# Kernel tuning notes

Measured on AMD Instinct MI355X. Metric: run time of the kernel, lower is better.

## Reference

```python
import jax, jax.numpy as jnp
import numpy as np

B = 50000      # batch of target nodes
N = 200000     # total nodes in feature table
K = 32         # sampled neighbors per node
F = 256        # feature dim
F_OUT = 256    # output dim


def setup_inputs() -> dict:
    key = jax.random.key(0)
    k1, k2, k3, k4, k5 = jax.random.split(key, 5)
    x_self = jax.random.normal(k1, (B, F), dtype=jnp.float32)
    feats = jax.random.normal(k2, (N, F), dtype=jnp.float32)
    neigh_idx = jax.random.randint(k3, (B, K), 0, N, dtype=jnp.int64)
    # Linear(2F -> F_OUT), stored as (in, out) for x @ W
    W = jax.random.normal(k4, (F_OUT, 2 * F), dtype=jnp.float32) * (1.0 / np.sqrt(2 * F))
    W = W.T  # (2F, F_OUT)
    b = jax.random.normal(k5, (F_OUT,), dtype=jnp.float32) * 0.01
    return {"x_self": x_self, "feats": feats, "neigh_idx": neigh_idx, "W": W, "b": b}


def reference(x_self, feats, neigh_idx, W, b):
    # gather neighbor features: [B, K, F]
    neigh_feats = feats[neigh_idx]
    # MeanAggregator: mean over neighbor axis (-2)
    x_neigh = neigh_feats.mean(axis=-2)            # [B, F]
    # concat=True path: cat([x_self, x_neigh], axis=1) -> [B, 2F]
    h = jnp.concatenate([x_self, x_neigh], axis=1)
    # Linear layer
    return h @ W + b                                # [B, F_OUT]
```

## Files before the change

### kernel.cpp

```cpp
#include <hip/hip_runtime.h>
#include <hip/hip_bf16.h>
#include <stdint.h>

#define NB 50000
#define NN 200000
#define KN 32
#define FD 256
#define F2 512
#define FO 256

typedef __attribute__((ext_vector_type(8))) short short8v;
typedef __attribute__((ext_vector_type(4))) short short4v;
typedef __attribute__((ext_vector_type(4))) float floatx4;
typedef __attribute__((ext_vector_type(2))) float float2v;

__device__ inline short f2bf(float f) {
    __hip_bfloat16 h = __float2bfloat16(f);
    return *reinterpret_cast<short*>(&h);
}

__global__ void k_quant_feats(const float* __restrict__ feats,
                              unsigned char* __restrict__ Q) {
    long t = (long)blockIdx.x * blockDim.x + threadIdx.x;
    long base = t * 8;
    const float4* src = (const float4*)(feats + base);
    float4 a = src[0], b = src[1];
    int lo = 0, hi = 0;
    lo = __builtin_amdgcn_cvt_pk_fp8_f32(a.x, a.y, lo, false);
    lo = __builtin_amdgcn_cvt_pk_fp8_f32(a.z, a.w, lo, true);
    hi = __builtin_amdgcn_cvt_pk_fp8_f32(b.x, b.y, hi, false);
    hi = __builtin_amdgcn_cvt_pk_fp8_f32(b.z, b.w, hi, true);
    int2 o = { lo, hi };
    *(int2*)(Q + base) = o;
}

__global__ void k_swizzle_W(const float* __restrict__ W,
                            __hip_bfloat16* __restrict__ Wsw) {
    int u = blockIdx.x * blockDim.x + threadIdx.x;
    if (u >= 16384) return;
    int l  = u & 63;
    int tl = (u >> 6) & 3;
    int c  = (u >> 8) & 15;
    int h  = (u >> 12) & 3;
    int n  = (h * 4 + tl) * 16 + (l & 15);
    int kb = c * 32 + (l >> 4) * 8;
    short o[8];
#pragma unroll
    for (int j = 0; j < 8; ++j)
        o[j] = f2bf(W[(long)(kb + j) * FO + n]);
    *(short8v*)((short*)Wsw + (long)u * 8) = *(short8v*)o;
}

__global__ void k_gather_mean(const unsigned char* __restrict__ Q,
                              const float* __restrict__ x_self,
                              const int* __restrict__ idx,
                              __hip_bfloat16* __restrict__ H) {
    int wave = threadIdx.x >> 6;
    int lane = threadIdx.x & 63;
    int b = blockIdx.x * 4 + wave;
    int c4 = lane * 4;

    float4 xs = *(const float4*)(x_self + (long)b * FD + c4);
    short so[4] = { f2bf(xs.x), f2bf(xs.y), f2bf(xs.z), f2bf(xs.w) };
    *(short4v*)((short*)H + (long)b * F2 + c4) = *(short4v*)so;

    const int* ib = idx + (long)b * KN;
    float ax = 0.f, ay = 0.f, az = 0.f, aw = 0.f;
#pragma unroll
    for (int k = 0; k < KN; ++k) {
        int id = ib[k];
        int v = *(const int*)(Q + (long)id * FD + c4);
        float2v lo = __builtin_amdgcn_cvt_pk_f32_fp8(v, false);
        float2v hi = __builtin_amdgcn_cvt_pk_f32_fp8(v, true);
        ax += lo.x; ay += lo.y; az += hi.x; aw += hi.y;
    }
    const float s = 1.0f / (float)KN;
    short o[4] = { f2bf(ax * s), f2bf(ay * s), f2bf(az * s), f2bf(aw * s) };
    *(short4v*)((short*)H + (long)b * F2 + FD + c4) = *(short4v*)o;
}

__global__ void __launch_bounds__(256, 2)
k_gemm(const __hip_bfloat16* __restrict__ H,
       const __hip_bfloat16* __restrict__ Wsw,
       const float* __restrict__ bias,
       float* __restrict__ out) {
    __shared__ char lB[64 * 1024];

    int tid  = threadIdx.x;
    int wave = tid >> 6;
    int lane = tid & 63;
    int cl   = lane & 15;
    int quad = lane >> 4;
    int kq   = quad * 8;

    int h  = blockIdx.x & 3;
    int rt = blockIdx.x >> 2;

    const char* gsrc = (const char*)Wsw + (long)h * 65536;
#pragma unroll
    for (int i = 0; i < 16; ++i) {
        int off = i * 4096 + wave * 1024;
        __builtin_amdgcn_global_load_lds(
            (__attribute__((address_space(1))) void*)(gsrc + off + lane * 16),
            (__attribute__((address_space(3))) void*)(lB + off),
            16, 0, 0);
    }
    __syncthreads();

    int mf = rt * 256 + wave * 64;

    floatx4 acc[4][4];
#pragma unroll
    for (int f = 0; f < 4; ++f)
#pragma unroll
        for (int t = 0; t < 4; ++t) acc[f][t] = (floatx4)(0.f);

    const short8v* lb = (const short8v*)lB;
    for (int c = 0; c < 16; ++c) {
        short8v a[4];
#pragma unroll
        for (int f = 0; f < 4; ++f) {
            long r = min(mf + f * 16 + cl, NB - 1);
            a[f] = *(const short8v*)((const short*)H + r * F2 + c * 32 + kq);
        }
#pragma unroll
        for (int t = 0; t < 4; ++t) {
            short8v bf = lb[(c * 4 + t) * 64 + lane];
#pragma unroll
            for (int f = 0; f < 4; ++f)
                acc[f][t] = __builtin_amdgcn_mfma_f32_16x16x32_bf16(a[f], bf, acc[f][t], 0, 0, 0);
        }
    }

#pragma unroll
    for (int t = 0; t < 4; ++t) {
        int n = h * 64 + t * 16 + cl;
        float bv = bias[n];
#pragma unroll
        for (int f = 0; f < 4; ++f) {
            int row = mf + f * 16 + quad * 4;
#pragma unroll
            for (int r = 0; r < 4; ++r) {
                if (row + r < NB)
                    out[(long)(row + r) * FO + n] = acc[f][t][r] + bv;
            }
        }
    }
}

extern "C" void kernel_launch(void* const* d_in, const int* in_sizes, int n_in,
                              void* d_out, int out_size, void* d_ws, size_t ws_size,
                              hipStream_t stream) {
    const float* x_self = (const float*)d_in[0];
    const float* feats  = (const float*)d_in[1];
    const int*   idx    = (const int*)d_in[2];
    const float* W      = (const float*)d_in[3];
    const float* bias   = (const float*)d_in[4];
    float* out = (float*)d_out;

    unsigned char*  Q   = (unsigned char*)d_ws;
    __hip_bfloat16* H   = (__hip_bfloat16*)((char*)d_ws + (size_t)NN * FD);
    __hip_bfloat16* Wsw = (__hip_bfloat16*)((char*)d_ws + (size_t)NN * FD
                                                        + (size_t)NB * F2 * 2);

    k_quant_feats<<<NN * FD / 8 / 256, 256, 0, stream>>>(feats, Q);
    k_swizzle_W<<<64, 256, 0, stream>>>(W, Wsw);
    k_gather_mean<<<NB / 4, 256, 0, stream>>>(Q, x_self, idx, H);
    k_gemm<<<4 * ((NB + 255) / 256), 256, 0, stream>>>(H, Wsw, bias, out);
}
```

Baseline: 440.3 us.

## Fuse x_self conversion into GEMM, widen gather loads, drop LDS weight staging

The gather kernel now writes only the neighbor-mean half in bf16. Each lane loads 16 fp8 bytes per neighbor across four neighbors in parallel, and the partial sums are reduced with cross-lane shuffles. The GEMM reads x_self in fp32 and converts it to bf16 inline, which removes the intermediate write and read of that half of H. Each 64-row block now covers all 256 output columns and streams the swizzled weights straight from global or cache instead of staging them in LDS. The cost is 128 accumulator registers per thread, less weight reuse per load, and repeated weight traffic through L2.

```diff
diff --git a/kernel.cpp b/kernel.cpp
--- a/kernel.cpp
+++ b/kernel.cpp
@@ -38,106 +38,127 @@
                             __hip_bfloat16* __restrict__ Wsw) {
     int u = blockIdx.x * blockDim.x + threadIdx.x;
     if (u >= 16384) return;
-    int l  = u & 63;
-    int tl = (u >> 6) & 3;
-    int c  = (u >> 8) & 15;
-    int h  = (u >> 12) & 3;
-    int n  = (h * 4 + tl) * 16 + (l & 15);
-    int kb = c * 32 + (l >> 4) * 8;
+    int c = u >> 10;
+    int t = (u >> 6) & 15;
+    int l = u & 63;
+    int kq = (l >> 4) * 8;
+    int n  = t * 16 + (l & 15);
     short o[8];
 #pragma unroll
     for (int j = 0; j < 8; ++j)
-        o[j] = f2bf(W[(long)(kb + j) * FO + n]);
+        o[j] = f2bf(W[(long)(c * 32 + kq + j) * FO + n]);
     *(short8v*)((short*)Wsw + (long)u * 8) = *(short8v*)o;
 }
 
 __global__ void k_gather_mean(const unsigned char* __restrict__ Q,
-                              const float* __restrict__ x_self,
                               const int* __restrict__ idx,
-                              __hip_bfloat16* __restrict__ H) {
+                              __hip_bfloat16* __restrict__ Hn) {
     int wave = threadIdx.x >> 6;
     int lane = threadIdx.x & 63;
     int b = blockIdx.x * 4 + wave;
-    int c4 = lane * 4;
-
-    float4 xs = *(const float4*)(x_self + (long)b * FD + c4);
-    short so[4] = { f2bf(xs.x), f2bf(xs.y), f2bf(xs.z), f2bf(xs.w) };
-    *(short4v*)((short*)H + (long)b * F2 + c4) = *(short4v*)so;
+    int cl   = lane & 15;
+    int quad = lane >> 4;
 
     const int* ib = idx + (long)b * KN;
-    float ax = 0.f, ay = 0.f, az = 0.f, aw = 0.f;
+    float2v acc2[8];
 #pragma unroll
-    for (int k = 0; k < KN; ++k) {
-        int id = ib[k];
-        int v = *(const int*)(Q + (long)id * FD + c4);
-        float2v lo = __builtin_amdgcn_cvt_pk_f32_fp8(v, false);
-        float2v hi = __builtin_amdgcn_cvt_pk_f32_fp8(v, true);
-        ax += lo.x; ay += lo.y; az += hi.x; aw += hi.y;
+    for (int j = 0; j < 8; ++j) acc2[j] = (float2v)(0.f);
+
+#pragma unroll
+    for (int k = 0; k < 8; ++k) {
+        int nid = ib[4 * k + quad];
+        int4 v = *(const int4*)(Q + (long)nid * FD + cl * 16);
+        acc2[0] += __builtin_amdgcn_cvt_pk_f32_fp8(v.x, false);
+        acc2[1] += __builtin_amdgcn_cvt_pk_f32_fp8(v.x, true);
+        acc2[2] += __builtin_amdgcn_cvt_pk_f32_fp8(v.y, false);
+        acc2[3] += __builtin_amdgcn_cvt_pk_f32_fp8(v.y, true);
+        acc2[4] += __builtin_amdgcn_cvt_pk_f32_fp8(v.z, false);
+        acc2[5] += __builtin_amdgcn_cvt_pk_f32_fp8(v.z, true);
+        acc2[6] += __builtin_amdgcn_cvt_pk_f32_fp8(v.w, false);
+        acc2[7] += __builtin_amdgcn_cvt_pk_f32_fp8(v.w, true);
     }
+
+#pragma unroll
+    for (int j = 0; j < 8; ++j) {
+        acc2[j].x += __shfl_xor(acc2[j].x, 16);
+        acc2[j].y += __shfl_xor(acc2[j].y, 16);
+        acc2[j].x += __shfl_xor(acc2[j].x, 32);
+        acc2[j].y += __shfl_xor(acc2[j].y, 32);
+    }
+
+    float2v p0 = (quad & 1) ? acc2[2] : acc2[0];
+    float2v p1 = (quad & 1) ? acc2[3] : acc2[1];
+    float2v q0 = (quad & 1) ? acc2[6] : acc2[4];
+    float2v q1 = (quad & 1) ? acc2[7] : acc2[5];
+    float2v s0 = (quad & 2) ? q0 : p0;
+    float2v s1 = (quad & 2) ? q1 : p1;
     const float s = 1.0f / (float)KN;
-    short o[4] = { f2bf(ax * s), f2bf(ay * s), f2bf(az * s), f2bf(aw * s) };
-    *(short4v*)((short*)H + (long)b * F2 + FD + c4) = *(short4v*)o;
+    short o[4] = { f2bf(s0.x * s), f2bf(s0.y * s), f2bf(s1.x * s), f2bf(s1.y * s) };
+    *(short4v*)((short*)Hn + (long)b * FD + cl * 16 + quad * 4) = *(short4v*)o;
 }
 
-__global__ void __launch_bounds__(256, 2)
-k_gemm(const __hip_bfloat16* __restrict__ H,
+__global__ void __launch_bounds__(128, 2)
+k_gemm(const float* __restrict__ x_self,
+       const __hip_bfloat16* __restrict__ Hn,
        const __hip_bfloat16* __restrict__ Wsw,
        const float* __restrict__ bias,
        float* __restrict__ out) {
-    __shared__ char lB[64 * 1024];
-
-    int tid  = threadIdx.x;
-    int wave = tid >> 6;
-    int lane = tid & 63;
+    int wave = threadIdx.x >> 6;
+    int lane = threadIdx.x & 63;
     int cl   = lane & 15;
     int quad = lane >> 4;
     int kq   = quad * 8;
 
-    int h  = blockIdx.x & 3;
-    int rt = blockIdx.x >> 2;
+    int mf = blockIdx.x * 64 + wave * 32;
+    long r0 = min(mf + cl, NB - 1);
+    long r1 = min(mf + 16 + cl, NB - 1);
 
-    const char* gsrc = (const char*)Wsw + (long)h * 65536;
+    floatx4 acc[2][16];
 #pragma unroll
-    for (int i = 0; i < 16; ++i) {
-        int off = i * 4096 + wave * 1024;
-        __builtin_amdgcn_global_load_lds(
-            (__attribute__((address_space(1))) void*)(gsrc + off + lane * 16),
-            (__attribute__((address_space(3))) void*)(lB + off),
-            16, 0, 0);
-    }
-    __syncthreads();
+    for (int f = 0; f < 2; ++f)
+#pragma unroll
+        for (int t = 0; t < 16; ++t) acc[f][t] = (floatx4)(0.f);
 
-    int mf = rt * 256 + wave * 64;
+    const short8v* wp = (const short8v*)Wsw;
 
-    floatx4 acc[4][4];
 #pragma unroll
-    for (int f = 0; f < 4; ++f)
+    for (int c = 0; c < 8; ++c) {
+        float4 p0 = *(const float4*)(x_self + r0 * FD + c * 32 + kq);
+        float4 p1 = *(const float4*)(x_self + r0 * FD + c * 32 + kq + 4);
+        float4 p2 = *(const float4*)(x_self + r1 * FD + c * 32 + kq);
+        float4 p3 = *(const float4*)(x_self + r1 * FD + c * 32 + kq + 4);
+        short a0s[8] = { f2bf(p0.x), f2bf(p0.y), f2bf(p0.z), f2bf(p0.w),
+                         f2bf(p1.x), f2bf(p1.y), f2bf(p1.z), f2bf(p1.w) };
+        short a1s[8] = { f2bf(p2.x), f2bf(p2.y), f2bf(p2.z), f2bf(p2.w),
+                         f2bf(p3.x), f2bf(p3.y), f2bf(p3.z), f2bf(p3.w) };
+        short8v a0 = *(short8v*)a0s;
+        short8v a1 = *(short8v*)a1s;
 #pragma unroll
-        for (int t = 0; t < 4; ++t) acc[f][t] = (floatx4)(0.f);
-
-    const short8v* lb = (const short8v*)lB;
-    for (int c = 0; c < 16; ++c) {
-        short8v a[4];
-#pragma unroll
-        for (int f = 0; f < 4; ++f) {
-            long r = min(mf + f * 16 + cl, NB - 1);
-            a[f] = *(const short8v*)((const short*)H + r * F2 + c * 32 + kq);
-        }
-#pragma unroll
-        for (int t = 0; t < 4; ++t) {
-            short8v bf = lb[(c * 4 + t) * 64 + lane];
-#pragma unroll
-            for (int f = 0; f < 4; ++f)
-                acc[f][t] = __builtin_amdgcn_mfma_f32_16x16x32_bf16(a[f], bf, acc[f][t], 0, 0, 0);
+        for (int t = 0; t < 16; ++t) {
+            short8v bf = wp[(c * 16 + t) * 64 + lane];
+            acc[0][t] = __builtin_amdgcn_mfma_f32_16x16x32_bf16(a0, bf, acc[0][t], 0, 0, 0);
+            acc[1][t] = __builtin_amdgcn_mfma_f32_16x16x32_bf16(a1, bf, acc[1][t], 0, 0, 0);
         }
     }
 
 #pragma unroll
-    for (int t = 0; t < 4; ++t) {
-        int n = h * 64 + t * 16 + cl;
+    for (int c = 0; c < 8; ++c) {
+        short8v a0 = *(const short8v*)((const short*)Hn + r0 * FD + c * 32 + kq);
+        short8v a1 = *(const short8v*)((const short*)Hn + r1 * FD + c * 32 + kq);
+#pragma unroll
+        for (int t = 0; t < 16; ++t) {
+            short8v bf = wp[((c + 8) * 16 + t) * 64 + lane];
+            acc[0][t] = __builtin_amdgcn_mfma_f32_16x16x32_bf16(a0, bf, acc[0][t], 0, 0, 0);
+            acc[1][t] = __builtin_amdgcn_mfma_f32_16x16x32_bf16(a1, bf, acc[1][t], 0, 0, 0);
+        }
+    }
+
+#pragma unroll
+    for (int t = 0; t < 16; ++t) {
+        int n = t * 16 + cl;
         float bv = bias[n];
 #pragma unroll
-        for (int f = 0; f < 4; ++f) {
+        for (int f = 0; f < 2; ++f) {
             int row = mf + f * 16 + quad * 4;
 #pragma unroll
             for (int r = 0; r < 4; ++r) {
@@ -159,12 +180,12 @@
     float* out = (float*)d_out;
 
     unsigned char*  Q   = (unsigned char*)d_ws;
-    __hip_bfloat16* H   = (__hip_bfloat16*)((char*)d_ws + (size_t)NN * FD);
+    __hip_bfloat16* Hn  = (__hip_bfloat16*)((char*)d_ws + (size_t)NN * FD);
     __hip_bfloat16* Wsw = (__hip_bfloat16*)((char*)d_ws + (size_t)NN * FD
-                                                        + (size_t)NB * F2 * 2);
+                                                        + (size_t)NB * FD * 2);
 
     k_quant_feats<<<NN * FD / 8 / 256, 256, 0, stream>>>(feats, Q);
     k_swizzle_W<<<64, 256, 0, stream>>>(W, Wsw);
-    k_gather_mean<<<NB / 4, 256, 0, stream>>>(Q, x_self, idx, H);
-    k_gemm<<<4 * ((NB + 255) / 256), 256, 0, stream>>>(H, Wsw, bias, out);
+    k_gather_mean<<<NB / 4, 256, 0, stream>>>(Q, idx, Hn);
+    k_gemm<<<(NB + 63) / 64, 128, 0, stream>>>(x_self, Hn, Wsw, bias, out);
 }
```

After: 429.1 us. -2.5%, faster.
